# Kernel tuning notes

Hardware: AMD Instinct MI355X
Metric: run time of the kernel (lower is better)

Reference implementation:

```python
import jax, jax.numpy as jnp
from jax import lax
import numpy as np

B, S, T = 64, 100, 96
SRC_V, PRIM_V, NPROD, NFLD = 32000, 16000, 201, 100
E, HE, H, F, ATT = 128, 128, 256, 64, 256
DIN = E + ATT + F + H  # 704 = action_emb + prev_att + field + parent_state


def setup_inputs():
    key = jax.random.key(0)
    ks = jax.random.split(key, 40)
    def p(k, shape):
        return (jax.random.normal(k, shape) * 0.05).astype(jnp.float32)
    sent_lens = jax.random.randint(ks[0], (B,), 1, S + 1)
    src_tokens = jax.random.randint(ks[1], (B, S), 0, SRC_V)
    prev_action_ids = jax.random.randint(ks[2], (B, T), 0, NPROD)
    frontier_ids = jax.random.randint(ks[3], (B, T), 0, NFLD)
    # parent_t[b, t] must point at an already-produced decoder state (< t)
    parent_t = jax.random.randint(ks[4], (B, T), 0, T) % jnp.maximum(jnp.arange(T), 1)
    atype = jax.random.randint(ks[5], (B, T), 0, 4)  # 0=apply,1=gen,2=copy,3=pad
    is_applyconstr = (atype == 0).astype(jnp.float32)
    is_gentoken = (atype == 1).astype(jnp.float32)
    is_copy = (atype == 2).astype(jnp.float32)
    is_copy_tok = (jax.random.uniform(ks[6], (B, T, S)) < 0.05).astype(jnp.float32) * is_copy[:, :, None]
    applyconstr_ids = jax.random.randint(ks[7], (B, T), 0, NPROD)
    gentok_ids = jax.random.randint(ks[8], (B, T), 0, PRIM_V)
    return dict(
        src_tokens=src_tokens, sent_lens=sent_lens, prev_action_ids=prev_action_ids,
        parent_t=parent_t, frontier_ids=frontier_ids, applyconstr_ids=applyconstr_ids,
        gentok_ids=gentok_ids, is_applyconstr=is_applyconstr, is_gentoken=is_gentoken,
        is_copy=is_copy, is_copy_tok=is_copy_tok,
        src_emb=p(ks[9], (SRC_V, E)), prod_emb=p(ks[10], (NPROD, E)),
        prim_emb=p(ks[11], (PRIM_V, E)), field_emb=p(ks[12], (NFLD, F)),
        Wih_f=p(ks[13], (4 * HE, E)), Whh_f=p(ks[14], (4 * HE, HE)), bih_f=p(ks[15], (4 * HE,)), bhh_f=p(ks[16], (4 * HE,)),
        Wih_b=p(ks[17], (4 * HE, E)), Whh_b=p(ks[18], (4 * HE, HE)), bih_b=p(ks[19], (4 * HE,)), bhh_b=p(ks[20], (4 * HE,)),
        Wih_d=p(ks[21], (4 * H, DIN)), Whh_d=p(ks[22], (4 * H, H)), bih_d=p(ks[23], (4 * H,)), bhh_d=p(ks[24], (4 * H,)),
        W_lin_attn=p(ks[25], (H, H)), W_att_vec=p(ks[26], (ATT, 2 * H)), W_ptr=p(ks[27], (ATT, H)),
        W_a2e=p(ks[28], (E, ATT)), W_gen=p(ks[29], (1, ATT)), b_gen=p(ks[30], (1,)),
    )


def _cell(x, h, c, Wih, Whh, bih, bhh):
    # torch.nn.LSTMCell gate order: i, f, g, o
    g = x @ Wih.T + bih + h @ Whh.T + bhh
    i, f, gg, o = jnp.split(g, 4, axis=-1)
    c = jax.nn.sigmoid(f) * c + jax.nn.sigmoid(i) * jnp.tanh(gg)
    return jax.nn.sigmoid(o) * jnp.tanh(c), c


def _forward(src_tokens, sent_lens, prev_action_ids, parent_t, frontier_ids,
             applyconstr_ids, gentok_ids, is_applyconstr, is_gentoken, is_copy, is_copy_tok,
             src_emb, prod_emb, prim_emb, field_emb,
             Wih_f, Whh_f, bih_f, bhh_f, Wih_b, Whh_b, bih_b, bhh_b,
             Wih_d, Whh_d, bih_d, bhh_d,
             W_lin_attn, W_att_vec, W_ptr, W_a2e, W_gen, b_gen):
    b, s = src_tokens.shape
    t_max = prev_action_ids.shape[1]
    emb = src_emb[src_tokens]                                  # [B,S,E]
    valid = jnp.arange(s)[None, :] < sent_lens[:, None]        # [B,S]

    def make_step(Wih, Whh, bih, bhh):
        def step(carry, xs):
            h, c = carry
            xt, vt = xs
            hn, cn = _cell(xt, h, c, Wih, Whh, bih, bhh)
            m = vt[:, None]
            hn = jnp.where(m, hn, h)
            cn = jnp.where(m, cn, c)
            return (hn, cn), hn
        return step

    z = jnp.zeros((b, HE), emb.dtype)
    (hf, cf), hs_f = lax.scan(make_step(Wih_f, Whh_f, bih_f, bhh_f), (z, z),
                              (emb.transpose(1, 0, 2), valid.T))
    (hb, cb), hs_b = lax.scan(make_step(Wih_b, Whh_b, bih_b, bhh_b), (z, z),
                              (emb[:, ::-1].transpose(1, 0, 2), valid[:, ::-1].T))
    hs_b = hs_b[::-1]                                          # re-align to forward order
    encodings = jnp.concatenate([hs_f, hs_b], -1).transpose(1, 0, 2) * valid[:, :, None]  # [B,S,H]
    h = jnp.concatenate([hf, hb], -1)                          # [B,H] final bi-state
    c = jnp.concatenate([cf, cb], -1)
    h_enc_final = h

    src_pad = ~valid
    enc_attn = encodings @ W_lin_attn.T                        # [B,S,H]

    def s_attention(hh):
        aw = jnp.einsum('bsh,bh->bs', enc_attn, hh)
        aw = jax.nn.softmax(jnp.where(src_pad, -jnp.inf, aw), axis=1)
        ctx = jnp.einsum('bs,bsh->bh', aw, encodings)
        return jnp.tanh(jnp.concatenate([ctx, hh], -1) @ W_att_vec.T)

    # decode step t = 0 with zero input
    h, c = _cell(jnp.zeros((b, DIN), emb.dtype), h, c, Wih_d, Whh_d, bih_d, bhh_d)
    buf = jnp.zeros((t_max, b, H), emb.dtype).at[0].set(h)     # states_sequence buffer
    s0 = s_attention(h)

    def dec_step(carry, xs):
        h, c, s_prev, buf = carry
        t, a_id, f_id, pt = xs
        parent = buf[pt, jnp.arange(b)]                        # data-dependent parent state
        inp = jnp.concatenate([prod_emb[a_id], s_prev, field_emb[f_id], parent], -1)
        h, c = _cell(inp, h, c, Wih_d, Whh_d, bih_d, bhh_d)
        buf = buf.at[t].set(h)
        s = s_attention(h)
        return (h, c, s, buf), s

    xs = (jnp.arange(1, t_max), prev_action_ids[:, 1:].T, frontier_ids[:, 1:].T, parent_t[:, 1:].T)
    _, s_rest = lax.scan(dec_step, (h, c, s0, buf), xs)
    s_att = jnp.concatenate([s0[None], s_rest], 0)             # [T,B,ATT]

    readout = s_att @ W_a2e.T                                  # [T,B,E]
    p_apply = jax.nn.softmax(jnp.einsum('tbe,ne->tbn', readout, prod_emb), axis=-1)
    p_tok = jax.nn.softmax(jnp.einsum('tbe,ve->tbv', readout, prim_emb), axis=-1)
    p_gen = jax.nn.sigmoid(s_att @ W_gen.T + b_gen)[..., 0]    # [T,B]
    hW = encodings @ W_ptr.T                                   # [B,S,ATT]
    sc = jnp.einsum('tbh,bsh->tbs', s_att, hW)
    p_copy_tok = jax.nn.softmax(jnp.where(src_pad[None], -jnp.inf, sc), axis=-1)

    tgt_copy = jnp.sum(p_copy_tok * is_copy_tok.transpose(1, 0, 2), axis=2)        # [T,B]
    tgt_apply = jnp.take_along_axis(p_apply, applyconstr_ids.T[:, :, None], axis=2)[..., 0]
    tgt_gen = jnp.take_along_axis(p_tok, gentok_ids.T[:, :, None], axis=2)[..., 0]

    ap = (tgt_apply * is_applyconstr.T
          + p_gen * tgt_gen * is_gentoken.T
          + (1.0 - p_gen) * tgt_copy * is_copy.T)
    pad = (is_applyconstr + is_gentoken + is_copy).T == 0
    ap = jnp.where(pad, 1e-7, ap)
    logp = jnp.log(ap) * (~pad)
    return jnp.sum(logp, axis=0), h_enc_final


def reference(src_tokens, sent_lens, prev_action_ids, parent_t, frontier_ids,
              applyconstr_ids, gentok_ids, is_applyconstr, is_gentoken, is_copy, is_copy_tok,
              src_emb, prod_emb, prim_emb, field_emb,
              Wih_f, Whh_f, bih_f, bhh_f, Wih_b, Whh_b, bih_b, bhh_b,
              Wih_d, Whh_d, bih_d, bhh_d,
              W_lin_attn, W_att_vec, W_ptr, W_a2e, W_gen, b_gen):
    return _forward(src_tokens, sent_lens, prev_action_ids, parent_t, frontier_ids,
                    applyconstr_ids, gentok_ids, is_applyconstr, is_gentoken, is_copy, is_copy_tok,
                    src_emb, prod_emb, prim_emb, field_emb,
                    Wih_f, Whh_f, bih_f, bhh_f, Wih_b, Whh_b, bih_b, bhh_b,
                    Wih_d, Whh_d, bih_d, bhh_d,
                    W_lin_attn, W_att_vec, W_ptr, W_a2e, W_gen, b_gen)
```

## Files before the change

kernel.cpp:

```cpp
#include <hip/hip_runtime.h>
#include <math.h>

typedef unsigned int uint;
typedef unsigned short ushort;
typedef unsigned char uchar;
typedef _Float16 v2h __attribute__((ext_vector_type(2)));
typedef short bf16x8 __attribute__((ext_vector_type(8)));
typedef float f32x4 __attribute__((ext_vector_type(4)));

__device__ __forceinline__ float sigf(float x) { return 1.f / (1.f + expf(-x)); }

__device__ __forceinline__ uint packh2(float a, float b) {
  v2h v; v[0] = (_Float16)a; v[1] = (_Float16)b;
  return __builtin_bit_cast(uint, v);
}
__device__ __forceinline__ ushort f2h(float x) {
  _Float16 h = (_Float16)x;
  return __builtin_bit_cast(ushort, h);
}
__device__ __forceinline__ float h2f(ushort u) {
  return (float)__builtin_bit_cast(_Float16, u);
}
__device__ __forceinline__ float dot2(uint w, uint x, float acc) {
  return __builtin_amdgcn_fdot2(__builtin_bit_cast(v2h, w), __builtin_bit_cast(v2h, x), acc, false);
}
__device__ __forceinline__ ushort f2bf(float f) {
  uint x = __builtin_bit_cast(uint, f);
  return (ushort)((x + 0x7fffu + ((x >> 16) & 1u)) >> 16);
}
__device__ __forceinline__ int dot8i4(uint w, uint x, int acc) {
#if __has_builtin(__builtin_amdgcn_sdot8)
  return __builtin_amdgcn_sdot8((int)w, (int)x, acc, false);
#else
#pragma unroll
  for (int j = 0; j < 8; j++) {
    int a = ((int)(w << (28 - 4 * j))) >> 28;
    int b = ((int)(x << (28 - 4 * j))) >> 28;
    acc += a * b;
  }
  return acc;
#endif
}
__device__ __forceinline__ char qi4b(float x) { return (char)(int)rintf(x * 7.f); }
__device__ __forceinline__ uint nib4(uint a) {
  a &= 0x0F0F0F0Fu;
  a |= a >> 4;
  a &= 0x00FF00FFu;
  a |= a >> 8;
  return a & 0xFFFFu;
}
__device__ __forceinline__ float rlf(float v, int l) {
  return __builtin_bit_cast(float, __builtin_amdgcn_readlane(__builtin_bit_cast(int, v), l));
}

__device__ __forceinline__ float wgval8(int k, int d, const float* Wih, const float* Whh) {
  if (k < 256) return Wih[d * 704 + 128 + k];
  if (k < 512) return Wih[d * 704 + 448 + (k - 256)];
  return Whh[d * 256 + (k - 512)];
}

__device__ __forceinline__ void tr_one(const float* __restrict__ src, float* __restrict__ dst,
                                       int i, int rows, int ld, int col0) {
  int r = i % rows, c = i / rows;
  dst[i] = src[r * ld + col0 + c];
}

__global__ __launch_bounds__(256) void k_prepack(
    const float* __restrict__ Wih_f, const float* __restrict__ Wih_b,
    const float* __restrict__ W_lin, const float* __restrict__ W_ptr,
    const float* __restrict__ W_att, const float* __restrict__ W_a2e,
    const float* __restrict__ Wih_d, const float* __restrict__ prim_emb,
    const float* __restrict__ bih_f, const float* __restrict__ bhh_f,
    const float* __restrict__ bih_b, const float* __restrict__ bhh_b,
    const float* __restrict__ bih_d, const float* __restrict__ bhh_d,
    const float* __restrict__ Whh_d,
    float* __restrict__ WIHFT, float* __restrict__ WIHBT, float* __restrict__ WLINT,
    float* __restrict__ WPTRT, float* __restrict__ WATTCT, float* __restrict__ WA2ET,
    float* __restrict__ WPRODT, float* __restrict__ WFLDT,
    uint* __restrict__ WAH16, ushort* __restrict__ PRIM16,
    float* __restrict__ BFB, float* __restrict__ BBB, float* __restrict__ BDD,
    float* __restrict__ DEN, uint* __restrict__ WG4, float* __restrict__ wscale) {
  __shared__ float arr[768];
  __shared__ float red[256];
  if (blockIdx.x >= 10332) {
    int d = blockIdx.x - 10332, tid = threadIdx.x;
    float v0 = wgval8(tid, d, Wih_d, Whh_d);
    float v1 = wgval8(tid + 256, d, Wih_d, Whh_d);
    float v2 = wgval8(tid + 512, d, Wih_d, Whh_d);
    arr[tid] = v0; arr[tid + 256] = v1; arr[tid + 512] = v2;
    red[tid] = fmaxf(fabsf(v0), fmaxf(fabsf(v1), fabsf(v2)));
    __syncthreads();
    for (int off = 128; off; off >>= 1) {
      if (tid < off) red[tid] = fmaxf(red[tid], red[tid + off]);
      __syncthreads();
    }
    float wmax = red[0];
    float inv = (wmax > 0.f) ? (7.f / wmax) : 0.f;
    if (tid < 96) {
      uint u = 0;
#pragma unroll
      for (int b = 0; b < 8; b++) {
        int q = (int)rintf(arr[8 * tid + b] * inv);
        u |= ((uint)q & 0xFu) << (4 * b);
      }
      WG4[((tid >> 2) * 1024 + d) * 4 + (tid & 3)] = u;
    }
    if (tid == 0) wscale[d] = wmax / 49.f;
    return;
  }
  int idx = blockIdx.x * 256 + threadIdx.x;
  if (idx < 65536) tr_one(Wih_f, WIHFT, idx, 512, 128, 0);
  else if (idx < 131072) tr_one(Wih_b, WIHBT, idx - 65536, 512, 128, 0);
  else if (idx < 196608) tr_one(W_lin, WLINT, idx - 131072, 256, 256, 0);
  else if (idx < 262144) tr_one(W_ptr, WPTRT, idx - 196608, 256, 256, 0);
  else if (idx < 327680) tr_one(W_att, WATTCT, idx - 262144, 256, 512, 0);
  else if (idx < 360448) tr_one(W_a2e, WA2ET, idx - 327680, 128, 256, 0);
  else if (idx < 491520) tr_one(Wih_d, WPRODT, idx - 360448, 1024, 704, 0);
  else if (idx < 557056) tr_one(Wih_d, WFLDT, idx - 491520, 1024, 704, 384);
  else if (idx < 589824) {
    int i2 = idx - 557056;
    int kk = i2 >> 8, r = i2 & 255;
    WAH16[i2] = packh2(W_att[r * 512 + 256 + 2 * kk], W_att[r * 512 + 257 + 2 * kk]);
  } else if (idx < 590848) {
    int i2 = idx - 589824;
    if (i2 < 512) { BFB[i2] = bih_f[i2] + bhh_f[i2]; BBB[i2] = bih_b[i2] + bhh_b[i2]; }
    BDD[i2] = bih_d[i2] + bhh_d[i2];
  } else if (idx < 596992) {
    DEN[idx - 590848] = 0.f;
  } else if (idx < 2644992) {
    int i2 = idx - 596992;
    PRIM16[i2] = f2bf(prim_emb[i2]);
  }
}

__global__ __launch_bounds__(256) void k_pfw2(
    const float* __restrict__ prod_emb, const float* __restrict__ field_emb,
    const float* __restrict__ WPRODT, const float* __restrict__ WFLDT,
    float* __restrict__ PW, float* __restrict__ FW) {
  int bi = blockIdx.x, tid = threadIdx.x;
  const float* emb; const float* WT; float* outp; int K, a;
  if (bi < 201) { a = bi; emb = prod_emb; WT = WPRODT; outp = PW; K = 128; }
  else { a = bi - 201; emb = field_emb; WT = WFLDT; outp = FW; K = 64; }
  __shared__ float es[128];
  if (tid < K) es[tid] = emb[a * K + tid];
  __syncthreads();
  float acc[4] = {0, 0, 0, 0};
  for (int k = 0; k < K; k++) {
    float ev = es[k];
#pragma unroll
    for (int j = 0; j < 4; j++) acc[j] = fmaf(ev, WT[k * 1024 + tid + j * 256], acc[j]);
  }
#pragma unroll
  for (int j = 0; j < 4; j++) outp[a * 1024 + tid + j * 256] = acc[j];
}

__global__ __launch_bounds__(256) void k_xproj2(const int* __restrict__ toks,
    const float* __restrict__ embt,
    const float* __restrict__ WTF, const float* __restrict__ WTB,
    const float* __restrict__ biasF, const float* __restrict__ biasB,
    float* __restrict__ outF, float* __restrict__ outB) {
  int bi = blockIdx.x;
  const float* WT = (bi < 400) ? WTF : WTB;
  const float* bias = (bi < 400) ? biasF : biasB;
  float* outp = (bi < 400) ? outF : outB;
  int row0 = (bi % 400) * 16;
  __shared__ __align__(16) float a[16][128];
  __shared__ int tk[16];
  int tid = threadIdx.x;
  if (tid < 16) {
    int row = row0 + tid;
    int b = row & 63, s = row >> 6;
    tk[tid] = toks[b * 100 + s];
  }
  __syncthreads();
#pragma unroll
  for (int i = 0; i < 8; i++) {
    int idx = tid + i * 256;
    int r = idx >> 7, k = idx & 127;
    a[r][k] = embt[tk[r] * 128 + k];
  }
  __syncthreads();
  int c = tid;
  float acc0[16], acc1[16];
  float b0 = bias[c], b1 = bias[c + 256];
#pragma unroll
  for (int r = 0; r < 16; r++) { acc0[r] = b0; acc1[r] = b1; }
  for (int k = 0; k < 128; k++) {
    float w0 = WT[k * 512 + c];
    float w1 = WT[k * 512 + c + 256];
#pragma unroll
    for (int r = 0; r < 16; r++) {
      float av = a[r][k];
      acc0[r] = fmaf(av, w0, acc0[r]);
      acc1[r] = fmaf(av, w1, acc1[r]);
    }
  }
#pragma unroll
  for (int r = 0; r < 16; r++) {
    outp[(row0 + r) * 512 + c] = acc0[r];
    outp[(row0 + r) * 512 + c + 256] = acc1[r];
  }
}

__global__ __launch_bounds__(512) void k_enc_scan(
    const float* __restrict__ xpf, const float* __restrict__ xpb,
    const float* __restrict__ WhhF, const float* __restrict__ WhhB,
    const int* __restrict__ lens,
    float* __restrict__ enc, float* __restrict__ h0, float* __restrict__ c0,
    float* __restrict__ outp) {
  int b = blockIdx.x & 63, dir = blockIdx.x >> 6;
  const float* xp = dir ? xpb : xpf;
  const float* Whh = dir ? WhhB : WhhF;
  int t = threadIdx.x;
  int lane = t & 63;
  float4 wv[32];
  {
    const float4* wr = (const float4*)(Whh + t * 128);
#pragma unroll
    for (int j = 0; j < 32; j++) wv[j] = wr[j];
  }
  __shared__ __align__(16) float hs[128];
  __shared__ float gs[512];
  float c = 0.f, hreg = 0.f;
  if (t < 128) hs[t] = 0.f;
  int len = lens[b];
  int pos0 = dir ? 99 : 0;
  float xv = xp[(pos0 * 64 + b) * 512 + t];
  __syncthreads();
  for (int s = 0; s < 100; s++) {
    int pos = dir ? (99 - s) : s;
    float hlo = hs[lane];
    float hhi = hs[64 + lane];
    int sn = (s < 99) ? s + 1 : 99;
    int posn = dir ? (99 - sn) : sn;
    float xnext = xp[(posn * 64 + b) * 512 + t];
    float a0 = xv, a1 = 0.f, a2 = 0.f, a3 = 0.f;
#pragma unroll
    for (int j = 0; j < 16; j++) {
      float4 w = wv[j];
      a0 = fmaf(w.x, rlf(hlo, 4 * j + 0), a0);
      a1 = fmaf(w.y, rlf(hlo, 4 * j + 1), a1);
      a2 = fmaf(w.z, rlf(hlo, 4 * j + 2), a2);
      a3 = fmaf(w.w, rlf(hlo, 4 * j + 3), a3);
    }
#pragma unroll
    for (int j = 0; j < 16; j++) {
      float4 w = wv[16 + j];
      a0 = fmaf(w.x, rlf(hhi, 4 * j + 0), a0);
      a1 = fmaf(w.y, rlf(hhi, 4 * j + 1), a1);
      a2 = fmaf(w.z, rlf(hhi, 4 * j + 2), a2);
      a3 = fmaf(w.w, rlf(hhi, 4 * j + 3), a3);
    }
    gs[t] = (a0 + a1) + (a2 + a3);
    __syncthreads();
    if (t < 128) {
      float ig = sigf(gs[t]);
      float fg = sigf(gs[128 + t]);
      float gg = tanhf(gs[256 + t]);
      float og = sigf(gs[384 + t]);
      float cn = fmaf(fg, c, ig * gg);
      float hn = og * tanhf(cn);
      if (pos < len) { c = cn; hreg = hn; }
      hs[t] = hreg;
      enc[(b * 100 + pos) * 256 + dir * 128 + t] = (pos < len) ? hreg : 0.f;
    }
    xv = xnext;
    __syncthreads();
  }
  if (t < 128) {
    h0[b * 256 + dir * 128 + t] = hreg;
    c0[b * 256 + dir * 128 + t] = c;
    outp[64 + b * 256 + dir * 128 + t] = hreg;
  }
}

__global__ __launch_bounds__(256) void k_proj2(
    const float* __restrict__ enc, const float* __restrict__ WlinT,
    const float* __restrict__ WptrT, const float* __restrict__ WattCT,
    ushort* __restrict__ eat16, ushort* __restrict__ hw16, ushort* __restrict__ ew16) {
  int bx = blockIdx.x;
  int which = bx >> 8;
  int b = (bx >> 2) & 63;
  int j0 = (bx & 3) * 64;
  const float* WT = (which == 0) ? WlinT : (which == 1) ? WptrT : WattCT;
  __shared__ __align__(16) float el[20][256];
  int tid = threadIdx.x;
  int jj = tid & 63, sg = tid >> 6;
  for (int st = 0; st < 5; st++) {
    __syncthreads();
#pragma unroll
    for (int i = 0; i < 20; i++) {
      int idx = tid + i * 256;
      int r = idx >> 8, k = idx & 255;
      el[r][k] = enc[(b * 100 + st * 20 + r) * 256 + k];
    }
    __syncthreads();
    float acc[5] = {0, 0, 0, 0, 0};
    for (int k4 = 0; k4 < 64; k4++) {
      float w0 = WT[(4 * k4 + 0) * 256 + j0 + jj];
      float w1 = WT[(4 * k4 + 1) * 256 + j0 + jj];
      float w2 = WT[(4 * k4 + 2) * 256 + j0 + jj];
      float w3 = WT[(4 * k4 + 3) * 256 + j0 + jj];
#pragma unroll
      for (int q = 0; q < 5; q++) {
        float4 ev = *(const float4*)&el[sg * 5 + q][4 * k4];
        acc[q] = fmaf(ev.x, w0, fmaf(ev.y, w1, fmaf(ev.z, w2, fmaf(ev.w, w3, acc[q]))));
      }
    }
#pragma unroll
    for (int q = 0; q < 5; q++) {
      int s = st * 20 + sg * 5 + q;
      ushort hv = f2h(acc[q]);
      if (which == 0) eat16[(b * 100 + s) * 256 + j0 + jj] = hv;
      else if (which == 1) hw16[(b * 100 + s) * 256 + j0 + jj] = hv;
      else ew16[(b * 100 + s) * 256 + j0 + jj] = hv;
    }
  }
}

__global__ __launch_bounds__(1024, 4) void k_decoder(
    const uint* __restrict__ WG4, const float* __restrict__ wscale,
    const uint* __restrict__ WAH16,
    const float* __restrict__ bdd, const float* __restrict__ PW, const float* __restrict__ FW,
    const float* __restrict__ h0g, const float* __restrict__ c0g,
    const uint* __restrict__ EAT32, const uint* __restrict__ EW32,
    const int* __restrict__ aid, const int* __restrict__ ptp, const int* __restrict__ fid,
    const int* __restrict__ lens, float* __restrict__ sbuf) {
  __shared__ __align__(16) uint ea[100 * 136];
  __shared__ __align__(16) uint ewl[100 * 128];
  __shared__ __align__(16) uint xq[32];
  __shared__ __align__(16) uint histn[96 * 32];
  __shared__ float gsm[1024];
  __shared__ float vp[4][256];
  __shared__ float aw[128];
  __shared__ __align__(16) uint hx32[128];
  __shared__ float csm[256];
  __shared__ __align__(16) char h0q[256];
  int e = blockIdx.x, tid = threadIdx.x;
  int len = lens[e];
  float bias0 = bdd[tid];
  float wsc = wscale[tid];
  for (int u = tid; u < 12800; u += 1024) {
    int s = u >> 7, kk = u & 127;
    ea[s * 136 + kk] = EAT32[(e * 100 + s) * 128 + kk];
    ewl[u] = EW32[e * 12800 + u];
  }
  if (tid < 256) {
    csm[tid] = c0g[e * 256 + tid];
    h0q[tid] = qi4b(h0g[e * 256 + tid]);
  }
  const uint4* wq = (const uint4*)WG4 + tid;
  uint4 wr[8];
#pragma unroll
  for (int qq = 0; qq < 8; qq++) wr[qq] = wq[qq * 1024];
  uint war[32];
  {
    int r_v = tid & 255, q_v = tid >> 8;
#pragma unroll
    for (int i = 0; i < 32; i++) war[i] = WAH16[(q_v * 32 + i) * 256 + r_v];
  }
  __syncthreads();
  if (tid < 32) {
    xq[tid] = 0u;
    const uint* p = (const uint*)&h0q[8 * tid];
    histn[tid] = nib4(p[0]) | (nib4(p[1]) << 16);
  }
  __syncthreads();
  int gacc;
  {
    int a0 = 0, a1 = 0, a2 = 0, a3 = 0;
#pragma unroll 4
    for (int qq = 16; qq < 24; qq++) {
      uint4 wv = wq[qq * 1024];
      uint4 xv = *(const uint4*)&histn[(qq - 16) * 4];
      a0 = dot8i4(wv.x, xv.x, a0);
      a1 = dot8i4(wv.y, xv.y, a1);
      a2 = dot8i4(wv.z, xv.z, a2);
      a3 = dot8i4(wv.w, xv.w, a3);
    }
    gacc = a0 + a1 + a2 + a3;
  }
  float pf = 0.f;
  for (int t = 0; t < 96; t++) {
    int tn = (t < 95) ? (t + 1) : 95;
    int ptn = ptp[e * 96 + tn];
    {
      int a0 = gacc, a1 = 0, a2 = 0, a3 = 0;
#pragma unroll
      for (int qq = 0; qq < 8; qq++) {
        uint4 xv = *(const uint4*)&xq[qq * 4];
        a0 = dot8i4(wr[qq].x, xv.x, a0);
        a1 = dot8i4(wr[qq].y, xv.y, a1);
        a2 = dot8i4(wr[qq].z, xv.z, a2);
        a3 = dot8i4(wr[qq].w, xv.w, a3);
      }
      gsm[tid] = fmaf((float)(a0 + a1 + a2 + a3), wsc, bias0 + pf);
    }
    __syncthreads();
    if (tid < 256) {
      int d = tid;
      float gi = gsm[d], gf = gsm[256 + d], gg = gsm[512 + d], go = gsm[768 + d];
      float c = fmaf(sigf(gf), csm[d], sigf(gi) * tanhf(gg));
      csm[d] = c;
      float h = sigf(go) * tanhf(c);
      float hp = __shfl_xor(h, 1);
      if (!(d & 1)) hx32[d >> 1] = packh2(h, hp);
      uint v = ((uint)(uchar)qi4b(h) & 0xFu) << (4 * (d & 7));
      v |= (uint)__shfl_xor((int)v, 1);
      v |= (uint)__shfl_xor((int)v, 2);
      v |= (uint)__shfl_xor((int)v, 4);
      if (!(d & 7)) histn[t * 32 + (d >> 3)] = v;
    }
    __syncthreads();
    {
      if (tid < 800) {
        int s = tid >> 3, sub = tid & 7;
        if (s < len) {
          const uint4* ep = (const uint4*)&ea[s * 136 + sub * 16];
          const uint4* hp = (const uint4*)&hx32[sub * 16];
          float a = 0.f;
#pragma unroll
          for (int i = 0; i < 4; i++) {
            uint4 ev = ep[i], hv = hp[i];
            a = dot2(ev.x, hv.x, a);
            a = dot2(ev.y, hv.y, a);
            a = dot2(ev.z, hv.z, a);
            a = dot2(ev.w, hv.w, a);
          }
          a += __shfl_down(a, 4);
          a += __shfl_down(a, 2);
          a += __shfl_down(a, 1);
          if (sub == 0) aw[s] = a;
        }
      }
      int a0 = 0, a1 = 0, a2 = 0, a3 = 0;
#pragma unroll 4
      for (int qq = 0; qq < 8; qq++) {
        uint4 wv = wq[(8 + qq) * 1024];
        uint4 xv = *(const uint4*)&histn[ptn * 32 + qq * 4];
        a0 = dot8i4(wv.x, xv.x, a0);
        a1 = dot8i4(wv.y, xv.y, a1);
        a2 = dot8i4(wv.z, xv.z, a2);
        a3 = dot8i4(wv.w, xv.w, a3);
      }
#pragma unroll 4
      for (int qq = 0; qq < 8; qq++) {
        uint4 wv = wq[(16 + qq) * 1024];
        uint4 xv = *(const uint4*)&histn[t * 32 + qq * 4];
        a0 = dot8i4(wv.x, xv.x, a0);
        a1 = dot8i4(wv.y, xv.y, a1);
        a2 = dot8i4(wv.z, xv.z, a2);
        a3 = dot8i4(wv.w, xv.w, a3);
      }
      gacc = a0 + a1 + a2 + a3;
    }
    __syncthreads();
    {
      int an = aid[e * 96 + tn], fn = fid[e * 96 + tn];
      float pw_n = PW[an * 1024 + tid];
      float fw_n = FW[fn * 1024 + tid];
      {
        int r = tid & 255, q = tid >> 8;
        float part = 0.f;
#pragma unroll
        for (int i = 0; i < 32; i++)
          part = dot2(war[i], hx32[q * 32 + i], part);
        vp[q][r] = part;
      }
      if (tid < 64) {
        float a0 = (tid < len) ? aw[tid] : -1e30f;
        float a1 = (64 + tid < len) ? aw[64 + tid] : -1e30f;
        float m = fmaxf(a0, a1);
#pragma unroll
        for (int off = 32; off; off >>= 1) m = fmaxf(m, __shfl_xor(m, off));
        float x0 = expf(a0 - m), x1 = expf(a1 - m);
        float ss = x0 + x1;
#pragma unroll
        for (int off = 32; off; off >>= 1) ss += __shfl_xor(ss, off);
        float rinv = 1.f / ss;
        aw[tid] = x0 * rinv;
        aw[64 + tid] = x1 * rinv;
      }
      pf = pw_n + fw_n;
    }
    __syncthreads();
    if (tid < 256) {
      int r = tid;
      const ushort* ew = (const ushort*)ewl;
      float c0 = 0.f, c1 = 0.f, c2 = 0.f, c3 = 0.f;
      for (int s = 0; s < 25; s++) {
        c0 = fmaf(aw[s], h2f(ew[s * 256 + r]), c0);
        c1 = fmaf(aw[25 + s], h2f(ew[(25 + s) * 256 + r]), c1);
        c2 = fmaf(aw[50 + s], h2f(ew[(50 + s) * 256 + r]), c2);
        c3 = fmaf(aw[75 + s], h2f(ew[(75 + s) * 256 + r]), c3);
      }
      float sv = tanhf((vp[0][r] + c0) + (vp[1][r] + c1) + (vp[2][r] + c2) + (vp[3][r] + c3));
      sbuf[(t * 64 + e) * 256 + r] = sv;
      uint v = ((uint)(uchar)qi4b(sv) & 0xFu) << (4 * (r & 7));
      v |= (uint)__shfl_xor((int)v, 1);
      v |= (uint)__shfl_xor((int)v, 2);
      v |= (uint)__shfl_xor((int)v, 4);
      if (!(r & 7)) xq[r >> 3] = v;
    }
    __syncthreads();
  }
}

__global__ __launch_bounds__(256) void k_readout(const float* __restrict__ sbuf,
    const float* __restrict__ wT, float* __restrict__ rd, ushort* __restrict__ rd16) {
  int row0 = blockIdx.x * 16;
  __shared__ __align__(16) float sl[16][256];
  int tid = threadIdx.x;
#pragma unroll
  for (int i = 0; i < 16; i++) {
    int idx = tid + i * 256;
    int r = idx >> 8, k = idx & 255;
    sl[r][k] = sbuf[(row0 + r) * 256 + k];
  }
  __syncthreads();
  int c = tid & 127, rg = tid >> 7;
  float acc[8] = {0, 0, 0, 0, 0, 0, 0, 0};
  for (int k4 = 0; k4 < 64; k4++) {
    float w0 = wT[(4 * k4 + 0) * 128 + c];
    float w1 = wT[(4 * k4 + 1) * 128 + c];
    float w2 = wT[(4 * k4 + 2) * 128 + c];
    float w3 = wT[(4 * k4 + 3) * 128 + c];
#pragma unroll
    for (int r = 0; r < 8; r++) {
      float4 s4 = *(const float4*)&sl[rg * 8 + r][4 * k4];
      acc[r] = fmaf(s4.x, w0, fmaf(s4.y, w1, fmaf(s4.z, w2, fmaf(s4.w, w3, acc[r]))));
    }
  }
#pragma unroll
  for (int r = 0; r < 8; r++) {
    int row = row0 + rg * 8 + r;
    rd[row * 128 + c] = acc[r];
    rd16[row * 128 + c] = f2bf(acc[r]);
  }
}

__global__ __launch_bounds__(256) void k_apply2(
    const float* __restrict__ rd, const float* __restrict__ prod,
    const int* __restrict__ ids, float* __restrict__ tga) {
  __shared__ __align__(16) float pl[201 * 128];
  __shared__ __align__(16) float rl[32][128];
  int tid = threadIdx.x;
  int row0 = blockIdx.x * 32;
  for (int u = tid; u < 201 * 128; u += 256) pl[u] = prod[u];
  for (int u = tid; u < 4096; u += 256) {
    int r = u >> 7, k = u & 127;
    rl[r][k] = rd[(row0 + r) * 128 + k];
  }
  __syncthreads();
  int wv = tid >> 6, l = tid & 63;
  float lg[8][4];
#pragma unroll
  for (int rr = 0; rr < 8; rr++)
#pragma unroll
    for (int s = 0; s < 4; s++) lg[rr][s] = 0.f;
  int nvalid = (l + 192 < 201) ? 4 : 3;
  for (int k4 = 0; k4 < 32; k4++) {
    float4 rv[8];
#pragma unroll
    for (int rr = 0; rr < 8; rr++) rv[rr] = *(const float4*)&rl[wv * 8 + rr][4 * k4];
#pragma unroll
    for (int s = 0; s < 4; s++) {
      if (s < nvalid) {
        float4 pv = *(const float4*)&pl[(l + 64 * s) * 128 + 4 * k4];
#pragma unroll
        for (int rr = 0; rr < 8; rr++)
          lg[rr][s] = fmaf(pv.x, rv[rr].x, fmaf(pv.y, rv[rr].y,
                      fmaf(pv.z, rv[rr].z, fmaf(pv.w, rv[rr].w, lg[rr][s]))));
      }
    }
  }
#pragma unroll
  for (int rr = 0; rr < 8; rr++) {
    float m = -1e30f;
#pragma unroll
    for (int s = 0; s < 4; s++) if (s < nvalid) m = fmaxf(m, lg[rr][s]);
#pragma unroll
    for (int off = 32; off; off >>= 1) m = fmaxf(m, __shfl_xor(m, off));
    float ss = 0.f;
#pragma unroll
    for (int s = 0; s < 4; s++) if (s < nvalid) ss += expf(lg[rr][s] - m);
#pragma unroll
    for (int off = 32; off; off >>= 1) ss += __shfl_xor(ss, off);
    int row = row0 + wv * 8 + rr;
    int tt = row >> 6, bb = row & 63;
    int id = ids[bb * 96 + tt];
    if (l == (id & 63)) {
      int s = id >> 6;
      tga[row] = expf(lg[rr][s] - m) / ss;
    }
  }
}

__global__ __launch_bounds__(256) void k_tok_den2(
    const ushort* __restrict__ rd16, const ushort* __restrict__ prim16,
    float* __restrict__ den) {
  int wave = threadIdx.x >> 6, lane = threadIdx.x & 63;
  int rowblk = blockIdx.x >> 3, strip = blockIdx.x & 7;
  int row0 = rowblk * 128 + wave * 32;
  int col0 = strip * 2000;
  int m = lane & 15, q = lane >> 4;
  bf16x8 a[2][4];
#pragma unroll
  for (int rg = 0; rg < 2; rg++)
#pragma unroll
    for (int i = 0; i < 4; i++)
      a[rg][i] = *(const bf16x8*)&rd16[(row0 + rg * 16 + m) * 128 + q * 8 + i * 32];
  float rs[2][4];
#pragma unroll
  for (int rg = 0; rg < 2; rg++)
#pragma unroll
    for (int r = 0; r < 4; r++) rs[rg][r] = 0.f;
  for (int ct = 0; ct < 125; ct++) {
    int cb = col0 + ct * 16 + m;
    f32x4 acc0 = {0.f, 0.f, 0.f, 0.f};
    f32x4 acc1 = {0.f, 0.f, 0.f, 0.f};
#pragma unroll
    for (int i = 0; i < 4; i++) {
      bf16x8 b = *(const bf16x8*)&prim16[cb * 128 + q * 8 + i * 32];
      acc0 = __builtin_amdgcn_mfma_f32_16x16x32_bf16(a[0][i], b, acc0, 0, 0, 0);
      acc1 = __builtin_amdgcn_mfma_f32_16x16x32_bf16(a[1][i], b, acc1, 0, 0, 0);
    }
#pragma unroll
    for (int r = 0; r < 4; r++) {
      rs[0][r] += expf(acc0[r]);
      rs[1][r] += expf(acc1[r]);
    }
  }
#pragma unroll
  for (int rg = 0; rg < 2; rg++)
#pragma unroll
    for (int r = 0; r < 4; r++) {
#pragma unroll
      for (int off = 1; off < 16; off <<= 1) rs[rg][r] += __shfl_xor(rs[rg][r], off);
    }
  if (m == 0) {
#pragma unroll
    for (int rg = 0; rg < 2; rg++)
#pragma unroll
      for (int r = 0; r < 4; r++)
        atomicAdd(&den[row0 + rg * 16 + q * 4 + r], rs[rg][r]);
  }
}

__global__ __launch_bounds__(256) void k_copy2f(
    const float* __restrict__ sbuf, const ushort* __restrict__ hw16,
    const float* __restrict__ ict, const int* __restrict__ lens,
    const float* __restrict__ rd, const float* __restrict__ prim,
    const float* __restrict__ wgen, const float* __restrict__ bgen,
    const int* __restrict__ gids, const float* __restrict__ den,
    const float* __restrict__ tga,
    const float* __restrict__ isap, const float* __restrict__ isgen,
    const float* __restrict__ iscp, float* __restrict__ outp) {
  __shared__ __align__(16) uint sx[96 * 128];
  __shared__ __align__(16) uint hw[100 * 132];
  __shared__ float sc[96 * 104];
  __shared__ __align__(16) uint wg16[128];
  __shared__ float tgcl[96];
  __shared__ float redf[256];
  int bb = blockIdx.x, tid = threadIdx.x;
  const uint* hwsrc = (const uint*)hw16;
  for (int u = tid; u < 12800; u += 256) {
    int s = u >> 7, kk = u & 127;
    hw[s * 132 + kk] = hwsrc[(bb * 100 + s) * 128 + kk];
  }
  for (int u = tid; u < 12288; u += 256) {
    int t = u >> 7, kk = u & 127;
    const float* p = &sbuf[(t * 64 + bb) * 256 + 2 * kk];
    sx[u] = packh2(p[0], p[1]);
  }
  if (tid < 128) wg16[tid] = packh2(wgen[2 * tid], wgen[2 * tid + 1]);
  __syncthreads();
  if (tid < 240) {
    int i = tid / 10, j = tid % 10;
    float acc[4][10] = {};
    for (int kk = 0; kk < 128; kk++) {
      uint hv[10], sv[4];
#pragma unroll
      for (int jj = 0; jj < 10; jj++) hv[jj] = hw[(j * 10 + jj) * 132 + kk];
#pragma unroll
      for (int ii = 0; ii < 4; ii++) sv[ii] = sx[(i * 4 + ii) * 128 + kk];
#pragma unroll
      for (int ii = 0; ii < 4; ii++)
#pragma unroll
        for (int jj = 0; jj < 10; jj++)
          acc[ii][jj] = dot2(sv[ii], hv[jj], acc[ii][jj]);
    }
#pragma unroll
    for (int ii = 0; ii < 4; ii++)
#pragma unroll
      for (int jj = 0; jj < 10; jj++)
        sc[(i * 4 + ii) * 104 + j * 10 + jj] = acc[ii][jj];
  }
  __syncthreads();
  int len = lens[bb];
  int wv = tid >> 6, l = tid & 63;
  for (int t = wv; t < 96; t += 4) {
    float a0 = (l < len) ? sc[t * 104 + l] : -1e30f;
    float a1 = -1e30f;
    if (l < 36 && 64 + l < len) a1 = sc[t * 104 + 64 + l];
    float m = fmaxf(a0, a1);
#pragma unroll
    for (int off = 32; off; off >>= 1) m = fmaxf(m, __shfl_xor(m, off));
    float x0 = expf(a0 - m), x1 = (l < 36) ? expf(a1 - m) : 0.f;
    float ss = x0 + x1;
#pragma unroll
    for (int off = 32; off; off >>= 1) ss += __shfl_xor(ss, off);
    float rinv = 1.f / ss;
    float w0 = x0 * rinv * ict[(bb * 96 + t) * 100 + l];
    float w1 = (l < 36) ? x1 * rinv * ict[(bb * 96 + t) * 100 + 64 + l] : 0.f;
    float tt = w0 + w1;
#pragma unroll
    for (int off = 32; off; off >>= 1) tt += __shfl_xor(tt, off);
    if (l == 0) tgcl[t] = tt;
  }
  __syncthreads();
  float lp = 0.f;
  if (tid < 96) {
    int t = tid, row = t * 64 + bb;
    float g = bgen[0];
    const uint* sxr = &sx[t * 128];
#pragma unroll 8
    for (int kk = 0; kk < 128; kk++) g = dot2(sxr[kk], wg16[kk], g);
    float pg = sigf(g);
    int gid = gids[bb * 96 + t];
    float l2 = 0.f;
    for (int k = 0; k < 128; k++) l2 = fmaf(rd[row * 128 + k], prim[gid * 128 + k], l2);
    float tgen = expf(l2) / den[row];
    float ia = isap[bb * 96 + t], ig = isgen[bb * 96 + t], ic = iscp[bb * 96 + t];
    float ap = tga[row] * ia + pg * tgen * ig + (1.f - pg) * tgcl[t] * ic;
    lp = (ia + ig + ic == 0.f) ? 0.f : logf(fmaxf(ap, 1e-30f));
  }
  redf[tid] = lp;
  __syncthreads();
#pragma unroll
  for (int off = 128; off > 0; off >>= 1) {
    if (tid < off) redf[tid] += redf[tid + off];
    __syncthreads();
  }
  if (tid == 0) outp[bb] = redf[0];
}

extern "C" void kernel_launch(void* const* d_in, const int* in_sizes, int n_in,
                              void* d_out, int out_size, void* d_ws, size_t ws_size,
                              hipStream_t stream) {
  const int* src_tokens = (const int*)d_in[0];
  const int* sent_lens = (const int*)d_in[1];
  const int* prev_action = (const int*)d_in[2];
  const int* parent_t = (const int*)d_in[3];
  const int* frontier = (const int*)d_in[4];
  const int* applyids = (const int*)d_in[5];
  const int* gentokids = (const int*)d_in[6];
  const float* is_ap = (const float*)d_in[7];
  const float* is_gen = (const float*)d_in[8];
  const float* is_cp = (const float*)d_in[9];
  const float* is_cp_tok = (const float*)d_in[10];
  const float* src_emb = (const float*)d_in[11];
  const float* prod_emb = (const float*)d_in[12];
  const float* prim_emb = (const float*)d_in[13];
  const float* field_emb = (const float*)d_in[14];
  const float* Wih_f = (const float*)d_in[15];
  const float* Whh_f = (const float*)d_in[16];
  const float* bih_f = (const float*)d_in[17];
  const float* bhh_f = (const float*)d_in[18];
  const float* Wih_b = (const float*)d_in[19];
  const float* Whh_b = (const float*)d_in[20];
  const float* bih_b = (const float*)d_in[21];
  const float* bhh_b = (const float*)d_in[22];
  const float* Wih_d = (const float*)d_in[23];
  const float* Whh_d = (const float*)d_in[24];
  const float* bih_d = (const float*)d_in[25];
  const float* bhh_d = (const float*)d_in[26];
  const float* W_lin = (const float*)d_in[27];
  const float* W_att = (const float*)d_in[28];
  const float* W_ptr = (const float*)d_in[29];
  const float* W_a2e = (const float*)d_in[30];
  const float* W_gen = (const float*)d_in[31];
  const float* b_gen = (const float*)d_in[32];
  float* out = (float*)d_out;
  float* w = (float*)d_ws;

  size_t o = 0;
  float* XPF = w + o; o += (size_t)100 * 64 * 512;
  float* XPB = w + o; o += (size_t)100 * 64 * 512;
  float* ENC = w + o; o += (size_t)64 * 100 * 256;
  float* H0 = w + o; o += 64 * 256;
  float* C0 = w + o; o += 64 * 256;
  float* WIHFT = w + o; o += 128 * 512;
  float* WIHBT = w + o; o += 128 * 512;
  float* WLINT = w + o; o += 256 * 256;
  float* WPTRT = w + o; o += 256 * 256;
  float* WATTCT = w + o; o += 256 * 256;
  float* WA2ET = w + o; o += 256 * 128;
  float* WPRODT = w + o; o += 128 * 1024;
  float* WFLDT = w + o; o += 64 * 1024;
  float* PW = w + o; o += (size_t)201 * 1024;
  float* FW = w + o; o += (size_t)100 * 1024;
  float* BFB = w + o; o += 512;
  float* BBB = w + o; o += 512;
  float* BDD = w + o; o += 1024;
  uint* WG4 = (uint*)(w + o); o += (size_t)24 * 4096;
  float* WSCALE = w + o; o += 1024;
  uint* WAH16 = (uint*)(w + o); o += 128 * 256;
  ushort* EAT16 = (ushort*)(w + o); o += (size_t)64 * 100 * 256 / 2;
  ushort* EW16 = (ushort*)(w + o); o += (size_t)64 * 100 * 256 / 2;
  ushort* HW16 = (ushort*)(w + o); o += (size_t)64 * 100 * 256 / 2;
  float* SBUF = w + o; o += (size_t)96 * 64 * 256;
  float* RDOUT = w + o; o += (size_t)96 * 64 * 128;
  ushort* RD16 = (ushort*)(w + o); o += (size_t)96 * 64 * 128 / 2 + 64;
  ushort* PRIM16 = (ushort*)(w + o); o += (size_t)16000 * 128 / 2 + 64;
  float* DEN = w + o; o += 6144;
  float* TGA = w + o; o += 6144;

  k_prepack<<<dim3(11356), dim3(256), 0, stream>>>(
      Wih_f, Wih_b, W_lin, W_ptr, W_att, W_a2e, Wih_d, prim_emb,
      bih_f, bhh_f, bih_b, bhh_b, bih_d, bhh_d, Whh_d,
      WIHFT, WIHBT, WLINT, WPTRT, WATTCT, WA2ET, WPRODT, WFLDT,
      WAH16, PRIM16, BFB, BBB, BDD, DEN, WG4, WSCALE);

  k_pfw2<<<dim3(301), dim3(256), 0, stream>>>(prod_emb, field_emb, WPRODT, WFLDT, PW, FW);

  k_xproj2<<<dim3(800), dim3(256), 0, stream>>>(src_tokens, src_emb, WIHFT, WIHBT,
                                                BFB, BBB, XPF, XPB);

  k_enc_scan<<<dim3(128), dim3(512), 0, stream>>>(XPF, XPB, Whh_f, Whh_b, sent_lens, ENC, H0, C0, out);

  k_proj2<<<dim3(768), dim3(256), 0, stream>>>(ENC, WLINT, WPTRT, WATTCT, EAT16, HW16, EW16);

  k_decoder<<<dim3(64), dim3(1024), 0, stream>>>(WG4, WSCALE, WAH16, BDD, PW, FW, H0, C0,
                                                 (const uint*)EAT16, (const uint*)EW16,
                                                 prev_action, parent_t, frontier, sent_lens,
                                                 SBUF);

  k_readout<<<dim3(384), dim3(256), 0, stream>>>(SBUF, WA2ET, RDOUT, RD16);
  k_apply2<<<dim3(192), dim3(256), 0, stream>>>(RDOUT, prod_emb, applyids, TGA);
  k_tok_den2<<<dim3(384), dim3(256), 0, stream>>>(RD16, PRIM16, DEN);
  k_copy2f<<<dim3(64), dim3(256), 0, stream>>>(SBUF, HW16, is_cp_tok, sent_lens,
                                               RDOUT, prim_emb, W_gen, b_gen, gentokids,
                                               DEN, TGA, is_ap, is_gen, is_cp, out);
}
```

Baseline: 1.242 ms.

## Interleave decoder LSTM gate rows so gate math uses lane shuffles

Decoder gate weight rows, scales, biases and the precomputed production/field projections are permuted so that the four gates (i, f, g, o) of each hidden unit sit in four adjacent threads. The cell update then gathers the gates with wavefront shuffles and keeps the cell state in a register. This removes the gate shared-memory buffer and one block-wide barrier per decoder timestep. In exchange, only one thread in four does the nonlinearity work, and every consumer of PW/FW/BDD must now agree on the interleaved layout.

```diff
diff --git a/kernel.cpp b/kernel.cpp
--- a/kernel.cpp
+++ b/kernel.cpp
@@ -84,6 +84,7 @@
   __shared__ float red[256];
   if (blockIdx.x >= 10332) {
     int d = blockIdx.x - 10332, tid = threadIdx.x;
+    int rn = (d & 255) * 4 + (d >> 8);
     float v0 = wgval8(tid, d, Wih_d, Whh_d);
     float v1 = wgval8(tid + 256, d, Wih_d, Whh_d);
     float v2 = wgval8(tid + 512, d, Wih_d, Whh_d);
@@ -103,9 +104,9 @@
         int q = (int)rintf(arr[8 * tid + b] * inv);
         u |= ((uint)q & 0xFu) << (4 * b);
       }
-      WG4[((tid >> 2) * 1024 + d) * 4 + (tid & 3)] = u;
-    }
-    if (tid == 0) wscale[d] = wmax / 49.f;
+      WG4[((tid >> 2) * 1024 + rn) * 4 + (tid & 3)] = u;
+    }
+    if (tid == 0) wscale[rn] = wmax / 49.f;
     return;
   }
   int idx = blockIdx.x * 256 + threadIdx.x;
@@ -124,7 +125,7 @@
   } else if (idx < 590848) {
     int i2 = idx - 589824;
     if (i2 < 512) { BFB[i2] = bih_f[i2] + bhh_f[i2]; BBB[i2] = bih_b[i2] + bhh_b[i2]; }
-    BDD[i2] = bih_d[i2] + bhh_d[i2];
+    BDD[(i2 & 255) * 4 + (i2 >> 8)] = bih_d[i2] + bhh_d[i2];
   } else if (idx < 596992) {
     DEN[idx - 590848] = 0.f;
   } else if (idx < 2644992) {
@@ -151,7 +152,7 @@
     for (int j = 0; j < 4; j++) acc[j] = fmaf(ev, WT[k * 1024 + tid + j * 256], acc[j]);
   }
 #pragma unroll
-  for (int j = 0; j < 4; j++) outp[a * 1024 + tid + j * 256] = acc[j];
+  for (int j = 0; j < 4; j++) outp[a * 1024 + tid * 4 + j] = acc[j];
 }
 
 __global__ __launch_bounds__(256) void k_xproj2(const int* __restrict__ toks,
@@ -330,11 +331,9 @@
   __shared__ __align__(16) uint ewl[100 * 128];
   __shared__ __align__(16) uint xq[32];
   __shared__ __align__(16) uint histn[96 * 32];
-  __shared__ float gsm[1024];
   __shared__ float vp[4][256];
   __shared__ float aw[128];
   __shared__ __align__(16) uint hx32[128];
-  __shared__ float csm[256];
   __shared__ __align__(16) char h0q[256];
   int e = blockIdx.x, tid = threadIdx.x;
   int len = lens[e];
@@ -345,10 +344,8 @@
     ea[s * 136 + kk] = EAT32[(e * 100 + s) * 128 + kk];
     ewl[u] = EW32[e * 12800 + u];
   }
-  if (tid < 256) {
-    csm[tid] = c0g[e * 256 + tid];
-    h0q[tid] = qi4b(h0g[e * 256 + tid]);
-  }
+  if (tid < 256) h0q[tid] = qi4b(h0g[e * 256 + tid]);
+  float creg = ((tid & 3) == 0) ? c0g[e * 256 + (tid >> 2)] : 0.f;
   const uint4* wq = (const uint4*)WG4 + tid;
   uint4 wr[8];
 #pragma unroll
@@ -394,22 +391,22 @@
         a2 = dot8i4(wr[qq].z, xv.z, a2);
         a3 = dot8i4(wr[qq].w, xv.w, a3);
       }
-      gsm[tid] = fmaf((float)(a0 + a1 + a2 + a3), wsc, bias0 + pf);
-    }
-    __syncthreads();
-    if (tid < 256) {
-      int d = tid;
-      float gi = gsm[d], gf = gsm[256 + d], gg = gsm[512 + d], go = gsm[768 + d];
-      float c = fmaf(sigf(gf), csm[d], sigf(gi) * tanhf(gg));
-      csm[d] = c;
-      float h = sigf(go) * tanhf(c);
-      float hp = __shfl_xor(h, 1);
-      if (!(d & 1)) hx32[d >> 1] = packh2(h, hp);
-      uint v = ((uint)(uchar)qi4b(h) & 0xFu) << (4 * (d & 7));
-      v |= (uint)__shfl_xor((int)v, 1);
-      v |= (uint)__shfl_xor((int)v, 2);
-      v |= (uint)__shfl_xor((int)v, 4);
-      if (!(d & 7)) histn[t * 32 + (d >> 3)] = v;
+      float g = fmaf((float)(a0 + a1 + a2 + a3), wsc, bias0 + pf);
+      float g1 = __shfl_xor(g, 1);
+      float g2 = __shfl_xor(g, 2);
+      float g3 = __shfl_xor(g, 3);
+      if ((tid & 3) == 0) {
+        int d = tid >> 2;
+        creg = fmaf(sigf(g1), creg, sigf(g) * tanhf(g2));
+        float h = sigf(g3) * tanhf(creg);
+        float hp = __shfl_xor(h, 4);
+        if (!(d & 1)) hx32[d >> 1] = packh2(h, hp);
+        uint v = ((uint)(uchar)qi4b(h) & 0xFu) << (4 * (d & 7));
+        v |= (uint)__shfl_xor((int)v, 4);
+        v |= (uint)__shfl_xor((int)v, 8);
+        v |= (uint)__shfl_xor((int)v, 16);
+        if (!(d & 7)) histn[t * 32 + (d >> 3)] = v;
+      }
     }
     __syncthreads();
     {
```

New measurement: 1.294 ms. 1.04x slower.

## Transpose attention-value matrix and use packed fp16 dot2 for context accumulation

Applied to the files above, without the earlier changes.

The projected encoder values are now written transposed (row index by output feature, then source position), so each decoder thread reads its own contiguous padded row from shared memory with 16-byte loads. The softmax weights are packed into fp16 pairs, and the context sum is computed with fdot2 instructions instead of scalar half-to-float conversions and FMAs. This shortens the per-step serial context computation inside the decoder recurrence. It lowers the precision of the attention weights to fp16 and adds zero padding plus shuffles for packing.

```diff
diff --git a/kernel.cpp b/kernel.cpp
--- a/kernel.cpp
+++ b/kernel.cpp
@@ -277,7 +277,7 @@
 __global__ __launch_bounds__(256) void k_proj2(
     const float* __restrict__ enc, const float* __restrict__ WlinT,
     const float* __restrict__ WptrT, const float* __restrict__ WattCT,
-    ushort* __restrict__ eat16, ushort* __restrict__ hw16, ushort* __restrict__ ew16) {
+    ushort* __restrict__ eat16, ushort* __restrict__ hw16, ushort* __restrict__ ewt16) {
   int bx = blockIdx.x;
   int which = bx >> 8;
   int b = (bx >> 2) & 63;
@@ -313,7 +313,7 @@
       ushort hv = f2h(acc[q]);
       if (which == 0) eat16[(b * 100 + s) * 256 + j0 + jj] = hv;
       else if (which == 1) hw16[(b * 100 + s) * 256 + j0 + jj] = hv;
-      else ew16[(b * 100 + s) * 256 + j0 + jj] = hv;
+      else ewt16[(b * 256 + j0 + jj) * 100 + s] = hv;
     }
   }
 }
@@ -323,16 +323,17 @@
     const uint* __restrict__ WAH16,
     const float* __restrict__ bdd, const float* __restrict__ PW, const float* __restrict__ FW,
     const float* __restrict__ h0g, const float* __restrict__ c0g,
-    const uint* __restrict__ EAT32, const uint* __restrict__ EW32,
+    const uint* __restrict__ EAT32, const uint* __restrict__ EWT32,
     const int* __restrict__ aid, const int* __restrict__ ptp, const int* __restrict__ fid,
     const int* __restrict__ lens, float* __restrict__ sbuf) {
   __shared__ __align__(16) uint ea[100 * 136];
-  __shared__ __align__(16) uint ewl[100 * 128];
+  __shared__ __align__(16) uint ewp[256 * 52];
   __shared__ __align__(16) uint xq[32];
   __shared__ __align__(16) uint histn[96 * 32];
   __shared__ float gsm[1024];
   __shared__ float vp[4][256];
   __shared__ float aw[128];
+  __shared__ __align__(16) uint aw2[56];
   __shared__ __align__(16) uint hx32[128];
   __shared__ float csm[256];
   __shared__ __align__(16) char h0q[256];
@@ -343,8 +344,10 @@
   for (int u = tid; u < 12800; u += 1024) {
     int s = u >> 7, kk = u & 127;
     ea[s * 136 + kk] = EAT32[(e * 100 + s) * 128 + kk];
-    ewl[u] = EW32[e * 12800 + u];
-  }
+    ewp[(u / 50) * 52 + (u % 50)] = EWT32[e * 12800 + u];
+  }
+  if (tid < 512) ewp[(tid >> 1) * 52 + 50 + (tid & 1)] = 0u;
+  if (tid < 6) aw2[50 + tid] = 0u;
   if (tid < 256) {
     csm[tid] = c0g[e * 256 + tid];
     h0q[tid] = qi4b(h0g[e * 256 + tid]);
@@ -478,23 +481,31 @@
 #pragma unroll
         for (int off = 32; off; off >>= 1) ss += __shfl_xor(ss, off);
         float rinv = 1.f / ss;
-        aw[tid] = x0 * rinv;
-        aw[64 + tid] = x1 * rinv;
+        float w0v = x0 * rinv, w1v = x1 * rinv;
+        if (tid < 32) {
+          aw2[tid] = packh2(__shfl(w0v, 2 * tid), __shfl(w0v, 2 * tid + 1));
+        } else if (tid < 50) {
+          int k = tid - 32;
+          aw2[tid] = packh2(__shfl(w1v, 2 * k), __shfl(w1v, 2 * k + 1));
+        }
       }
       pf = pw_n + fw_n;
     }
     __syncthreads();
     if (tid < 256) {
       int r = tid;
-      const ushort* ew = (const ushort*)ewl;
-      float c0 = 0.f, c1 = 0.f, c2 = 0.f, c3 = 0.f;
-      for (int s = 0; s < 25; s++) {
-        c0 = fmaf(aw[s], h2f(ew[s * 256 + r]), c0);
-        c1 = fmaf(aw[25 + s], h2f(ew[(25 + s) * 256 + r]), c1);
-        c2 = fmaf(aw[50 + s], h2f(ew[(50 + s) * 256 + r]), c2);
-        c3 = fmaf(aw[75 + s], h2f(ew[(75 + s) * 256 + r]), c3);
-      }
-      float sv = tanhf((vp[0][r] + c0) + (vp[1][r] + c1) + (vp[2][r] + c2) + (vp[3][r] + c3));
+      const uint4* ep4 = (const uint4*)&ewp[r * 52];
+      float c0 = 0.f, c1 = 0.f;
+#pragma unroll
+      for (int i = 0; i < 13; i++) {
+        uint4 ev = ep4[i];
+        uint4 wv4 = *(const uint4*)&aw2[4 * i];
+        c0 = dot2(ev.x, wv4.x, c0);
+        c1 = dot2(ev.y, wv4.y, c1);
+        c0 = dot2(ev.z, wv4.z, c0);
+        c1 = dot2(ev.w, wv4.w, c1);
+      }
+      float sv = tanhf((vp[0][r] + vp[1][r]) + (vp[2][r] + vp[3][r]) + (c0 + c1));
       sbuf[(t * 64 + e) * 256 + r] = sv;
       uint v = ((uint)(uchar)qi4b(sv) & 0xFu) << (4 * (r & 7));
       v |= (uint)__shfl_xor((int)v, 1);
@@ -807,7 +818,7 @@
   float* WSCALE = w + o; o += 1024;
   uint* WAH16 = (uint*)(w + o); o += 128 * 256;
   ushort* EAT16 = (ushort*)(w + o); o += (size_t)64 * 100 * 256 / 2;
-  ushort* EW16 = (ushort*)(w + o); o += (size_t)64 * 100 * 256 / 2;
+  ushort* EWT16 = (ushort*)(w + o); o += (size_t)64 * 100 * 256 / 2;
   ushort* HW16 = (ushort*)(w + o); o += (size_t)64 * 100 * 256 / 2;
   float* SBUF = w + o; o += (size_t)96 * 64 * 256;
   float* RDOUT = w + o; o += (size_t)96 * 64 * 128;
@@ -829,10 +840,10 @@
 
   k_enc_scan<<<dim3(128), dim3(512), 0, stream>>>(XPF, XPB, Whh_f, Whh_b, sent_lens, ENC, H0, C0, out);
 
-  k_proj2<<<dim3(768), dim3(256), 0, stream>>>(ENC, WLINT, WPTRT, WATTCT, EAT16, HW16, EW16);
+  k_proj2<<<dim3(768), dim3(256), 0, stream>>>(ENC, WLINT, WPTRT, WATTCT, EAT16, HW16, EWT16);
 
   k_decoder<<<dim3(64), dim3(1024), 0, stream>>>(WG4, WSCALE, WAH16, BDD, PW, FW, H0, C0,
-                                                 (const uint*)EAT16, (const uint*)EW16,
+                                                 (const uint*)EAT16, (const uint*)EWT16,
                                                  prev_action, parent_t, frontier, sent_lens,
                                                  SBUF);
 
```

Result: faster. 1.112 ms (-10.5%).
